# Kernel tuning notes

Measured on AMD Instinct MI355X. Metric: run time of the kernel, lower is better.

## Reference

```python
import jax, jax.numpy as jnp
import numpy as np

N_STREAMS = 4
SINKHORN_ITERS = 20
EPS = 1e-8


def sinkhorn_knopp(log_mat, num_iters=SINKHORN_ITERS, eps=EPS):
    mat = jnp.exp(log_mat)
    def body(_, m):
        m = m / (m.sum(axis=-2, keepdims=True) + eps)
        m = m / (m.sum(axis=-1, keepdims=True) + eps)
        return m
    return jax.lax.fori_loop(0, num_iters, body, mat)


def setup_inputs() -> dict:
    key = jax.random.key(0)
    B, L, C = 4, 2048, 1024
    n = N_STREAMS
    hidden = 4 * C
    ks = jax.random.split(key, 8)
    def xavier(k, shape):
        fan_in, fan_out = shape[0], shape[1]
        lim = np.sqrt(6.0 / (fan_in + fan_out))
        return jax.random.uniform(k, shape, jnp.float32, -lim, lim)
    return {
        "x": jax.random.normal(ks[0], (B, L, C), jnp.float32),
        "rms_weight": jnp.ones((C * n,), jnp.float32),
        "W_dyn": xavier(ks[1], (C * n, n * n + 2 * n)),  # Linear no-bias, stored [in,out]
        "bias_pre": jnp.zeros((1, n), jnp.float32),
        "bias_post": jnp.zeros((1, n), jnp.float32),
        "bias_res": jnp.zeros((n, n), jnp.float32),
        "alpha_pre": jnp.full((1,), 0.01, jnp.float32),
        "alpha_post": jnp.full((1,), 0.01, jnp.float32),
        "alpha_res": jnp.full((1,), 0.01, jnp.float32),
        "W1": xavier(ks[2], (C, hidden)),
        "b1": jnp.zeros((hidden,), jnp.float32),
        "W2": xavier(ks[3], (hidden, C)),
        "b2": jnp.zeros((C,), jnp.float32),
        "Wout": xavier(ks[4], (C * n, C)),
        "bout": jnp.zeros((C,), jnp.float32),
    }


def reference(x, rms_weight, W_dyn, bias_pre, bias_post, bias_res,
              alpha_pre, alpha_post, alpha_res, W1, b1, W2, b2, Wout, bout):
    B, L, C = x.shape
    n = bias_pre.shape[1]
    # x expanded across streams (broadcast view, no copy)
    x_exp = jnp.broadcast_to(x[:, :, None, :], (B, L, n, C))  # [B,L,n,C]
    x_flat = x_exp.reshape(B, L, n * C)
    # RMSNorm
    rms = jnp.sqrt(jnp.mean(x_flat * x_flat, axis=-1, keepdims=True) + EPS)
    x_norm = x_flat / rms * rms_weight
    # dynamic projection
    dynamic = x_norm @ W_dyn  # [B,L,n*n+2n]
    dyn_pre = dynamic[..., :n]
    dyn_post = dynamic[..., n:2 * n]
    dyn_res = dynamic[..., 2 * n:].reshape(B, L, n, n)
    H_pre = jax.nn.sigmoid(alpha_pre * dyn_pre + bias_pre)            # [B,L,n]
    H_post = 2.0 * jax.nn.sigmoid(alpha_post * dyn_post + bias_post)  # [B,L,n]
    H_res = sinkhorn_knopp(alpha_res * dyn_res + bias_res)            # [B,L,n,n]
    # pre-mix streams then residual MLP
    pre_mixed = jnp.einsum('bln,blnc->blc', H_pre, x_exp)
    h = jax.nn.gelu(pre_mixed @ W1 + b1, approximate=False)
    f_out = h @ W2 + b2  # [B,L,C]
    # post mixing + doubly-stochastic residual mixing
    post_mixed = H_post[..., None] * f_out[:, :, None, :]             # [B,L,n,C]
    res_mixed = jnp.einsum('blnm,blmc->blnc', H_res, x_exp)
    merged = (res_mixed + post_mixed).reshape(B, L, n * C)
    return merged @ Wout + bout + x
```

## Files before the change

### kernel.cpp

```cpp
#include <hip/hip_runtime.h>

typedef unsigned short u16;
typedef __bf16 bf16x8 __attribute__((ext_vector_type(8)));
typedef float f32x4 __attribute__((ext_vector_type(4)));

__device__ __forceinline__ u16 f2bf(float f) {
  unsigned int u = __builtin_bit_cast(unsigned int, f);
  u += 0x7fffu + ((u >> 16) & 1u);
  return (u16)(u >> 16);
}

__device__ __forceinline__ void gload_lds16(const u16* g, u16* l) {
  __builtin_amdgcn_global_load_lds((const __attribute__((address_space(1))) unsigned int*)g,
                                   (__attribute__((address_space(3))) unsigned int*)l,
                                   16, 0, 0);
}


__global__ __launch_bounds__(256) void weff_kernel(const float* __restrict__ rmsw,
                                                   const float* __restrict__ Wdyn,
                                                   float* __restrict__ WT) {
  int idx = blockIdx.x * 256 + threadIdx.x;
  int j = idx >> 10, c = idx & 1023;
  float s = 0.f;
#pragma unroll
  for (int st = 0; st < 4; ++st) {
    int r = st * 1024 + c;
    s += rmsw[r] * Wdyn[(long)r * 24 + j];
  }
  WT[idx] = s;
}

__global__ __launch_bounds__(256) void pack_weight(const float* __restrict__ W,
                                                   u16* __restrict__ FMB,
                                                   const int N, const int KC) {
  const long gid = (long)blockIdx.x * 256 + threadIdx.x;
  const int n = (int)(gid % N);
  const int k0 = (int)(gid / N) * 8;
  unsigned int p[4];
#pragma unroll
  for (int d = 0; d < 4; ++d) {
    const float lo = W[(long)(k0 + 2 * d) * N + n];
    const float hi = W[(long)(k0 + 2 * d + 1) * N + n];
    p[d] = (unsigned)f2bf(lo) | ((unsigned)f2bf(hi) << 16);
  }
  const long ad = ((long)(n >> 4) * KC + (k0 >> 5)) * 512 +
                  ((n & 15) + (((k0 >> 3) & 3) << 4)) * 8;
  *(uint4*)(FMB + ad) = make_uint4(p[0], p[1], p[2], p[3]);
}

__global__ __launch_bounds__(256) void prep_tokens(
    const float* __restrict__ x, const float* __restrict__ WT,
    const float* __restrict__ bias_pre, const float* __restrict__ bias_post,
    const float* __restrict__ bias_res, const float* __restrict__ a_pre,
    const float* __restrict__ a_post, const float* __restrict__ a_res,
    u16* __restrict__ preA, float* __restrict__ scal) {
  const int t = blockIdx.x;
  const int tid = threadIdx.x;
  const float4 xv = *(const float4*)(x + (long)t * 1024 + tid * 4);
  float ssq = xv.x * xv.x + xv.y * xv.y + xv.z * xv.z + xv.w * xv.w;
  float raw[24];
#pragma unroll
  for (int j = 0; j < 24; ++j) {
    const float4 w = *(const float4*)(WT + (long)j * 1024 + tid * 4);
    raw[j] = xv.x * w.x + xv.y * w.y + xv.z * w.z + xv.w * w.w;
  }
#pragma unroll
  for (int m = 1; m < 64; m <<= 1) {
    ssq += __shfl_xor(ssq, m);
#pragma unroll
    for (int j = 0; j < 24; ++j) raw[j] += __shfl_xor(raw[j], m);
  }
  __shared__ float red[4][25];
  __shared__ float tot[25];
  const int lane = tid & 63, wv = tid >> 6;
  if (lane == 0) {
#pragma unroll
    for (int j = 0; j < 24; ++j) red[wv][j] = raw[j];
    red[wv][24] = ssq;
  }
  __syncthreads();
  if (tid < 25) tot[tid] = red[0][tid] + red[1][tid] + red[2][tid] + red[3][tid];
  __syncthreads();

  const float rms = sqrtf(tot[24] * (1.0f / 1024.0f) + 1e-8f);
  const float rinv = 1.0f / rms;

  const float ap = a_pre[0];
  float s_pre = 0.f;
#pragma unroll
  for (int i = 0; i < 4; ++i)
    s_pre += 1.f / (1.f + expf(-(ap * tot[i] * rinv + bias_pre[i])));

  unsigned int lo = (unsigned)f2bf(s_pre * xv.x) | ((unsigned)f2bf(s_pre * xv.y) << 16);
  unsigned int hi = (unsigned)f2bf(s_pre * xv.z) | ((unsigned)f2bf(s_pre * xv.w) << 16);
  const int c0 = tid * 4;
  const long pa = ((long)(t >> 4) * 32 + (c0 >> 5)) * 512 +
                  ((t & 15) + (((c0 >> 3) & 3) << 4)) * 8 + (c0 & 7);
  *(uint2*)(preA + pa) = make_uint2(lo, hi);

  if (tid < 16) {
    const float ar = a_res[0];
    float Mv = expf(ar * tot[8 + tid] * rinv + bias_res[tid]);
#pragma unroll
    for (int it = 0; it < 20; ++it) {
      float cs = Mv + __shfl_xor(Mv, 4);
      cs += __shfl_xor(cs, 8);
      Mv = Mv / (cs + 1e-8f);
      float rs = Mv + __shfl_xor(Mv, 1);
      rs += __shfl_xor(rs, 2);
      Mv = Mv / (rs + 1e-8f);
    }
    float rs = Mv + __shfl_xor(Mv, 1);
    rs += __shfl_xor(rs, 2);
    if ((tid & 3) == 0) scal[(long)t * 8 + (tid >> 2)] = rs;
  }
  if (tid < 4) {
    const float apo = a_post[0];
    float hp = 2.f / (1.f + expf(-(apo * tot[4 + tid] * rinv + bias_post[tid])));
    scal[(long)t * 8 + 4 + tid] = hp;
  }
}

template <int EPI>
__global__ __launch_bounds__(256, 4) void gemm_fm(const u16* __restrict__ A,
                                                  const u16* __restrict__ B,
                                                  const int KCtot, const int GX,
                                                  const int N, const int KCout,
                                                  const float* __restrict__ bias,
                                                  const float* __restrict__ X,
                                                  const float* __restrict__ scal,
                                                  void* __restrict__ dstv) {
  const int tid = threadIdx.x;
  const int lane = tid & 63;
  const int wave = tid >> 6;
  const int wm = wave >> 1, wn = wave & 1;
  const int b = blockIdx.x;
  const int c = b & 7;
  const int s = b >> 3;
  const int bx = s % GX;
  const int by = c * 8 + s / GX;

  __shared__ u16 lds[2][16][512];

  const u16* gb[4];
  u16* lc[4];
#pragma unroll
  for (int l = 0; l < 4; ++l) {
    const int t = wave * 4 + l;
    gb[l] = (t < 8) ? (A + (long)(by * 8 + t) * KCtot * 512 + lane * 8)
                    : (B + (long)(bx * 8 + (t - 8)) * KCtot * 512 + lane * 8);
    lc[l] = &lds[0][t][0];
  }

#define STAGE(buf, kt)                                             \
  {                                                                \
    const long ko = (long)(kt)*512;                                \
    _Pragma("unroll") for (int l = 0; l < 4; ++l)                  \
        gload_lds16(gb[l] + ko, lc[l] + (buf)*8192);               \
  }

  f32x4 acc[4][4] = {};

  STAGE(0, 0);
  __syncthreads();

  for (int kt = 0; kt < KCtot; ++kt) {
    const int cur = kt & 1;
    if (kt + 1 < KCtot) STAGE(cur ^ 1, kt + 1);
    bf16x8 af[4], bfr[4];
#pragma unroll
    for (int i = 0; i < 4; ++i) {
      af[i] = *(const bf16x8*)&lds[cur][wm * 4 + i][lane * 8];
      bfr[i] = *(const bf16x8*)&lds[cur][8 + wn * 4 + i][lane * 8];
    }
#pragma unroll
    for (int i = 0; i < 4; ++i)
#pragma unroll
      for (int j = 0; j < 4; ++j)
        acc[i][j] = __builtin_amdgcn_mfma_f32_16x16x32_bf16(af[i], bfr[j], acc[i][j], 0, 0, 0);
    __syncthreads();
  }
#undef STAGE

  u16* ep = ((u16*)lds) + wave * 4096;

  if constexpr (EPI == 0) {
    u16* dst = (u16*)dstv;
#pragma unroll
    for (int i = 0; i < 4; ++i)
#pragma unroll
      for (int j = 0; j < 4; ++j) {
        const int col = bx * 128 + wn * 64 + j * 16 + (lane & 15);
        const float bcol = bias[col];
#pragma unroll
        for (int r = 0; r < 4; ++r) {
          const float v = acc[i][j][r] + bcol;
          const float g = 0.5f * v * (1.0f + erff(v * 0.70710678118654752f));
          const int lp = ((lane >> 4) * 4 + r) | ((((j & 1) << 1) | ((lane & 15) >> 3)) << 4);
          ep[(i * 2 + (j >> 1)) * 512 + lp * 8 + (lane & 7)] = f2bf(g);
        }
      }
    __syncthreads();
#pragma unroll
    for (int ch = 0; ch < 8; ++ch) {
      const int i = ch >> 1, jc = ch & 1;
      const long row16 = by * 8 + wm * 4 + i;
      const long col32 = bx * 4 + wn * 2 + jc;
      *(uint4*)(dst + (row16 * KCout + col32) * 512 + lane * 8) =
          *(const uint4*)(ep + ch * 512 + lane * 8);
    }
  } else if constexpr (EPI == 1) {
    u16* dst = (u16*)dstv;
#pragma unroll
    for (int i = 0; i < 4; ++i) {
      float rr[4][4], hh[4][4];
#pragma unroll
      for (int r = 0; r < 4; ++r) {
        const int row = by * 128 + wm * 64 + i * 16 + (lane >> 4) * 4 + r;
        const float4 rv = *(const float4*)(scal + (long)row * 8);
        const float4 hv = *(const float4*)(scal + (long)row * 8 + 4);
        rr[r][0] = rv.x; rr[r][1] = rv.y; rr[r][2] = rv.z; rr[r][3] = rv.w;
        hh[r][0] = hv.x; hh[r][1] = hv.y; hh[r][2] = hv.z; hh[r][3] = hv.w;
      }
#pragma unroll
      for (int jc = 0; jc < 2; ++jc) {
        __syncthreads();
#pragma unroll
        for (int jj = 0; jj < 2; ++jj) {
          const int j = jc * 2 + jj;
          const int col = bx * 128 + wn * 64 + j * 16 + (lane & 15);
          const float bcol = bias[col];
#pragma unroll
          for (int r = 0; r < 4; ++r) {
            const int row = by * 128 + wm * 64 + i * 16 + (lane >> 4) * 4 + r;
            const float f = acc[i][j][r] + bcol;
            const float xval = X[(long)row * 1024 + col];
            const int lp = ((lane >> 4) * 4 + r) | (((jj << 1) | ((lane & 15) >> 3)) << 4);
#pragma unroll
            for (int ss = 0; ss < 4; ++ss)
              ep[ss * 512 + lp * 8 + (lane & 7)] = f2bf(rr[r][ss] * xval + hh[r][ss] * f);
          }
        }
        __syncthreads();
        const long row16 = by * 8 + wm * 4 + i;
        const long col32 = bx * 4 + wn * 2 + jc;
#pragma unroll
        for (int ss = 0; ss < 4; ++ss)
          *(uint4*)(dst + (row16 * 128 + (long)ss * 32 + col32) * 512 + lane * 8) =
              *(const uint4*)(ep + ss * 512 + lane * 8);
      }
    }
  } else {
    float* dst = (float*)dstv;
    float* ep32 = (float*)ep;
#pragma unroll
    for (int half = 0; half < 2; ++half) {
      __syncthreads();
#pragma unroll
      for (int i2 = 0; i2 < 2; ++i2) {
        const int i = half * 2 + i2;
#pragma unroll
        for (int j = 0; j < 4; ++j) {
          const int col = bx * 128 + wn * 64 + j * 16 + (lane & 15);
          const float bcol = bias[col];
#pragma unroll
          for (int r = 0; r < 4; ++r) {
            const long row = by * 128 + wm * 64 + i * 16 + (lane >> 4) * 4 + r;
            ep32[(i2 * 16 + (lane >> 4) * 4 + r) * 64 + j * 16 + (lane & 15)] =
                acc[i][j][r] + bcol + X[row * 1024 + col];
          }
        }
      }
      __syncthreads();
#pragma unroll
      for (int q = 0; q < 8; ++q) {
        const int lr = q * 4 + (lane >> 4);
        const long row = by * 128 + wm * 64 + half * 32 + lr;
        const long col = bx * 128 + wn * 64 + (lane & 15) * 4;
        *(float4*)(dst + row * 1024 + col) =
            *(const float4*)(ep32 + lr * 64 + (lane & 15) * 4);
      }
    }
  }
}

extern "C" void kernel_launch(void* const* d_in, const int* in_sizes, int n_in,
                              void* d_out, int out_size, void* d_ws, size_t ws_size,
                              hipStream_t stream) {
  (void)in_sizes; (void)n_in; (void)out_size; (void)ws_size;
  const float* x = (const float*)d_in[0];
  const float* rmsw = (const float*)d_in[1];
  const float* Wdyn = (const float*)d_in[2];
  const float* bias_pre = (const float*)d_in[3];
  const float* bias_post = (const float*)d_in[4];
  const float* bias_res = (const float*)d_in[5];
  const float* a_pre = (const float*)d_in[6];
  const float* a_post = (const float*)d_in[7];
  const float* a_res = (const float*)d_in[8];
  const float* W1 = (const float*)d_in[9];
  const float* b1 = (const float*)d_in[10];
  const float* W2 = (const float*)d_in[11];
  const float* b2 = (const float*)d_in[12];
  const float* Wout = (const float*)d_in[13];
  const float* bout = (const float*)d_in[14];
  float* out = (float*)d_out;
  char* ws = (char*)d_ws;

  constexpr size_t MB = 1048576;
  u16* W1fm = (u16*)(ws);
  u16* W2fm = (u16*)(ws + 8 * MB);
  u16* WOfm = (u16*)(ws + 16 * MB);
  float* WT = (float*)(ws + 24 * MB);
  float* scal = (float*)(ws + 24 * MB + 98304);
  u16* h = (u16*)(ws + 25 * MB);
  u16* merged = (u16*)(ws + 89 * MB);
  u16* preA = (u16*)(ws + 89 * MB);

  weff_kernel<<<96, 256, 0, stream>>>(rmsw, Wdyn, WT);
  pack_weight<<<2048, 256, 0, stream>>>(W1, W1fm, 4096, 32);
  pack_weight<<<2048, 256, 0, stream>>>(W2, W2fm, 1024, 128);
  pack_weight<<<2048, 256, 0, stream>>>(Wout, WOfm, 1024, 128);
  prep_tokens<<<8192, 256, 0, stream>>>(x, WT, bias_pre, bias_post, bias_res,
                                        a_pre, a_post, a_res, preA, scal);
  gemm_fm<0><<<2048, 256, 0, stream>>>(preA, W1fm, 32, 32, 4096, 128, b1, nullptr, nullptr, h);
  gemm_fm<1><<<512, 256, 0, stream>>>(h, W2fm, 128, 8, 1024, 128, b2, x, scal, merged);
  gemm_fm<2><<<512, 256, 0, stream>>>(merged, WOfm, 128, 8, 1024, 0, bout, x, nullptr, out);
}
```

Measured before the change: 475.3 us.

## Merge weight packing launches, batch 16 tokens per prep block, fast erf GELU

The three pack_weight launches become one pack_all kernel that uses shift/mask indexing. prep_tokens now handles 16 tokens per 512-thread block: the projection and norm partials are reduced through shared memory instead of wave shuffles, and the bf16 preA tile is written with coalesced 16-byte stores. The GELU epilogue of the first GEMM replaces erff with an Abramowitz-Stegun polynomial using a fast reciprocal and __expf. The aims are lower launch overhead, less shuffle work, and cheaper epilogue math. The price is roughly 1e-7 absolute error in erf and a large shared-memory footprint in prep_tokens.

Result: faster. 431.1 us (-9.3%).

```diff
diff --git a/kernel.cpp b/kernel.cpp
--- a/kernel.cpp
+++ b/kernel.cpp
@@ -14,6 +14,20 @@
   __builtin_amdgcn_global_load_lds((const __attribute__((address_space(1))) unsigned int*)g,
                                    (__attribute__((address_space(3))) unsigned int*)l,
                                    16, 0, 0);
+}
+
+__device__ __forceinline__ float gelu_erf(float v) {
+  const float z = v * 0.70710678118654752f;
+  const float az = fabsf(z);
+  const float t = __builtin_amdgcn_rcpf(1.0f + 0.3275911f * az);
+  const float p = t * (0.254829592f +
+                  t * (-0.284496736f +
+                  t * (1.421413741f +
+                  t * (-1.453152027f + t * 1.061405429f))));
+  const float e = __expf(-az * az);
+  float er = 1.0f - p * e;
+  er = (z < 0.f) ? -er : er;
+  return 0.5f * v * (1.0f + er);
 }
 
 
@@ -31,12 +45,24 @@
   WT[idx] = s;
 }
 
-__global__ __launch_bounds__(256) void pack_weight(const float* __restrict__ W,
-                                                   u16* __restrict__ FMB,
-                                                   const int N, const int KC) {
-  const long gid = (long)blockIdx.x * 256 + threadIdx.x;
-  const int n = (int)(gid % N);
-  const int k0 = (int)(gid / N) * 8;
+__global__ __launch_bounds__(256) void pack_all(const float* __restrict__ W1,
+                                                const float* __restrict__ W2,
+                                                const float* __restrict__ WO,
+                                                u16* __restrict__ F1,
+                                                u16* __restrict__ F2,
+                                                u16* __restrict__ FO) {
+  const int blk = blockIdx.x;
+  const int sel = blk >> 11;
+  const float* W;
+  u16* FMB;
+  int lgN, KC;
+  if (sel == 0)      { W = W1; FMB = F1; lgN = 12; KC = 32; }
+  else if (sel == 1) { W = W2; FMB = F2; lgN = 10; KC = 128; }
+  else               { W = WO; FMB = FO; lgN = 10; KC = 128; }
+  const long gid = (long)(blk & 2047) * 256 + threadIdx.x;
+  const int N = 1 << lgN;
+  const int n = (int)(gid & (N - 1));
+  const int k0 = (int)(gid >> lgN) * 8;
   unsigned int p[4];
 #pragma unroll
   for (int d = 0; d < 4; ++d) {
@@ -49,59 +75,76 @@
   *(uint4*)(FMB + ad) = make_uint4(p[0], p[1], p[2], p[3]);
 }
 
-__global__ __launch_bounds__(256) void prep_tokens(
+__global__ __launch_bounds__(512) void prep_tokens(
     const float* __restrict__ x, const float* __restrict__ WT,
     const float* __restrict__ bias_pre, const float* __restrict__ bias_post,
     const float* __restrict__ bias_res, const float* __restrict__ a_pre,
     const float* __restrict__ a_post, const float* __restrict__ a_res,
     u16* __restrict__ preA, float* __restrict__ scal) {
-  const int t = blockIdx.x;
   const int tid = threadIdx.x;
-  const float4 xv = *(const float4*)(x + (long)t * 1024 + tid * 4);
-  float ssq = xv.x * xv.x + xv.y * xv.y + xv.z * xv.z + xv.w * xv.w;
-  float raw[24];
-#pragma unroll
-  for (int j = 0; j < 24; ++j) {
-    const float4 w = *(const float4*)(WT + (long)j * 1024 + tid * 4);
-    raw[j] = xv.x * w.x + xv.y * w.y + xv.z * w.z + xv.w * w.w;
-  }
-#pragma unroll
-  for (int m = 1; m < 64; m <<= 1) {
-    ssq += __shfl_xor(ssq, m);
-#pragma unroll
-    for (int j = 0; j < 24; ++j) raw[j] += __shfl_xor(raw[j], m);
-  }
-  __shared__ float red[4][25];
-  __shared__ float tot[25];
-  const int lane = tid & 63, wv = tid >> 6;
-  if (lane == 0) {
-#pragma unroll
-    for (int j = 0; j < 24; ++j) red[wv][j] = raw[j];
-    red[wv][24] = ssq;
+  const int b = blockIdx.x;
+  const long t0 = (long)b * 16;
+
+  __shared__ float red[32][16][26];
+  __shared__ float tot2[16][26];
+  __shared__ float spre[16];
+
+  {
+    const int tt = tid & 15;
+    const int cc = tid >> 4;
+    const float* xp = x + (t0 + tt) * 1024 + cc * 32;
+    float part[25];
+#pragma unroll
+    for (int j = 0; j < 25; ++j) part[j] = 0.f;
+#pragma unroll
+    for (int g = 0; g < 8; ++g) {
+      const float4 xv = *(const float4*)(xp + g * 4);
+      part[24] += xv.x * xv.x + xv.y * xv.y + xv.z * xv.z + xv.w * xv.w;
+#pragma unroll
+      for (int j = 0; j < 24; ++j) {
+        const float4 wv = *(const float4*)(WT + (long)j * 1024 + cc * 32 + g * 4);
+        part[j] += xv.x * wv.x + xv.y * wv.y + xv.z * wv.z + xv.w * wv.w;
+      }
+    }
+#pragma unroll
+    for (int j = 0; j < 25; ++j) red[cc][tt][j] = part[j];
   }
   __syncthreads();
-  if (tid < 25) tot[tid] = red[0][tid] + red[1][tid] + red[2][tid] + red[3][tid];
+
+  {
+    const int tt = tid >> 5;
+    const int j = tid & 31;
+    if (j < 25) {
+      float s = 0.f;
+#pragma unroll
+      for (int cc = 0; cc < 32; ++cc) s += red[cc][tt][j];
+      tot2[tt][j] = s;
+    }
+  }
   __syncthreads();
 
-  const float rms = sqrtf(tot[24] * (1.0f / 1024.0f) + 1e-8f);
-  const float rinv = 1.0f / rms;
-
-  const float ap = a_pre[0];
-  float s_pre = 0.f;
-#pragma unroll
-  for (int i = 0; i < 4; ++i)
-    s_pre += 1.f / (1.f + expf(-(ap * tot[i] * rinv + bias_pre[i])));
-
-  unsigned int lo = (unsigned)f2bf(s_pre * xv.x) | ((unsigned)f2bf(s_pre * xv.y) << 16);
-  unsigned int hi = (unsigned)f2bf(s_pre * xv.z) | ((unsigned)f2bf(s_pre * xv.w) << 16);
-  const int c0 = tid * 4;
-  const long pa = ((long)(t >> 4) * 32 + (c0 >> 5)) * 512 +
-                  ((t & 15) + (((c0 >> 3) & 3) << 4)) * 8 + (c0 & 7);
-  *(uint2*)(preA + pa) = make_uint2(lo, hi);
-
-  if (tid < 16) {
+  if (tid < 256) {
+    const int tt = tid >> 4;
+    const int m = tid & 15;
+    const long t = t0 + tt;
+    const float rms = sqrtf(tot2[tt][24] * (1.0f / 1024.0f) + 1e-8f);
+    const float rinv = 1.0f / rms;
+
+    if (m == 0) {
+      const float ap = a_pre[0];
+      float s_pre = 0.f;
+#pragma unroll
+      for (int i = 0; i < 4; ++i)
+        s_pre += 1.f / (1.f + expf(-(ap * tot2[tt][i] * rinv + bias_pre[i])));
+      spre[tt] = s_pre;
+    }
+    if (m < 4) {
+      const float apo = a_post[0];
+      float hp = 2.f / (1.f + expf(-(apo * tot2[tt][4 + m] * rinv + bias_post[m])));
+      scal[t * 8 + 4 + m] = hp;
+    }
     const float ar = a_res[0];
-    float Mv = expf(ar * tot[8 + tid] * rinv + bias_res[tid]);
+    float Mv = expf(ar * tot2[tt][8 + m] * rinv + bias_res[m]);
 #pragma unroll
     for (int it = 0; it < 20; ++it) {
       float cs = Mv + __shfl_xor(Mv, 4);
@@ -113,12 +156,28 @@
     }
     float rs = Mv + __shfl_xor(Mv, 1);
     rs += __shfl_xor(rs, 2);
-    if ((tid & 3) == 0) scal[(long)t * 8 + (tid >> 2)] = rs;
-  }
-  if (tid < 4) {
-    const float apo = a_post[0];
-    float hp = 2.f / (1.f + expf(-(apo * tot[4 + tid] * rinv + bias_post[tid])));
-    scal[(long)t * 8 + 4 + tid] = hp;
+    if ((m & 3) == 0) scal[t * 8 + (m >> 2)] = rs;
+  }
+  __syncthreads();
+
+  {
+    const int w = tid >> 6;
+    const int lane = tid & 63;
+    const int tl = lane & 15;
+    const int co = (lane >> 4) * 8;
+    const float sp = spre[tl];
+#pragma unroll
+    for (int p = 0; p < 4; ++p) {
+      const int ki = p * 8 + w;
+      const float* xr = x + (t0 + tl) * 1024 + ki * 32 + co;
+      const float4 xa = *(const float4*)(xr);
+      const float4 xb = *(const float4*)(xr + 4);
+      unsigned q0 = (unsigned)f2bf(sp * xa.x) | ((unsigned)f2bf(sp * xa.y) << 16);
+      unsigned q1 = (unsigned)f2bf(sp * xa.z) | ((unsigned)f2bf(sp * xa.w) << 16);
+      unsigned q2 = (unsigned)f2bf(sp * xb.x) | ((unsigned)f2bf(sp * xb.y) << 16);
+      unsigned q3 = (unsigned)f2bf(sp * xb.z) | ((unsigned)f2bf(sp * xb.w) << 16);
+      *(uint4*)(preA + ((long)b * 32 + ki) * 512 + lane * 8) = make_uint4(q0, q1, q2, q3);
+    }
   }
 }
 
@@ -195,8 +254,7 @@
         const float bcol = bias[col];
 #pragma unroll
         for (int r = 0; r < 4; ++r) {
-          const float v = acc[i][j][r] + bcol;
-          const float g = 0.5f * v * (1.0f + erff(v * 0.70710678118654752f));
+          const float g = gelu_erf(acc[i][j][r] + bcol);
           const int lp = ((lane >> 4) * 4 + r) | ((((j & 1) << 1) | ((lane & 15) >> 3)) << 4);
           ep[(i * 2 + (j >> 1)) * 512 + lp * 8 + (lane & 7)] = f2bf(g);
         }
@@ -318,11 +376,9 @@
   u16* preA = (u16*)(ws + 89 * MB);
 
   weff_kernel<<<96, 256, 0, stream>>>(rmsw, Wdyn, WT);
-  pack_weight<<<2048, 256, 0, stream>>>(W1, W1fm, 4096, 32);
-  pack_weight<<<2048, 256, 0, stream>>>(W2, W2fm, 1024, 128);
-  pack_weight<<<2048, 256, 0, stream>>>(Wout, WOfm, 1024, 128);
-  prep_tokens<<<8192, 256, 0, stream>>>(x, WT, bias_pre, bias_post, bias_res,
-                                        a_pre, a_post, a_res, preA, scal);
+  pack_all<<<6144, 256, 0, stream>>>(W1, W2, Wout, W1fm, W2fm, WOfm);
+  prep_tokens<<<512, 512, 0, stream>>>(x, WT, bias_pre, bias_post, bias_res,
+                                       a_pre, a_post, a_res, preA, scal);
   gemm_fm<0><<<2048, 256, 0, stream>>>(preA, W1fm, 32, 32, 4096, 128, b1, nullptr, nullptr, h);
   gemm_fm<1><<<512, 256, 0, stream>>>(h, W2fm, 128, 8, 1024, 128, b2, x, scal, merged);
   gemm_fm<2><<<512, 256, 0, stream>>>(merged, WOfm, 128, 8, 1024, 0, bout, x, nullptr, out);
```
